# Performance work log

Measured on AMD Instinct MI355X. Metric: run time of the kernel, lower is better.

Reference implementation:

```python
import jax, jax.numpy as jnp
import numpy as np

S, B, D = 512, 256, 256

def _gelu(x):
    return jax.nn.gelu(x, approximate=False)  # torch nn.GELU default is exact erf

def _blacket(a, b, bl_w, bl_b):
    # GELU(Linear(cat([a,b], -1))); torch Linear: x @ W.T + b
    return _gelu(jnp.concatenate([a, b], axis=-1) @ bl_w.T + bl_b)

def setup_inputs() -> dict:
    key = jax.random.key(0)
    k1, k2, k3, k4, k5 = jax.random.split(key, 5)
    return {
        "src": jax.random.normal(k1, (S, B, D), dtype=jnp.float32),
        "map_w": jax.random.normal(k2, (D, D), dtype=jnp.float32) * (1.0 / np.sqrt(D)),
        "map_b": jax.random.normal(k3, (D,), dtype=jnp.float32) * 0.02,
        "bl_w": jax.random.normal(k4, (D, 2 * D), dtype=jnp.float32) * (1.0 / np.sqrt(2 * D)),
        "bl_b": jax.random.normal(k5, (D,), dtype=jnp.float32) * 0.02,
    }

def reference(src, map_w, map_b, bl_w, bl_b):
    # map_first: src <- GELU(Linear(src))
    h = _gelu(src @ map_w.T + map_b)          # [S, B, D]
    # base lie_func: x = h[i-1] (zeros at i=0), y = h[i]
    x = jnp.concatenate([jnp.zeros_like(h[:1]), h[:-1]], axis=0)
    delta = x + _blacket(x, h, bl_w, bl_b)    # [S, B, D]
    # jacobi identity for i >= 2 (note: torch `r += J` aliases context in base
    # mode, so J is folded into the carried context -> cumulative effect)
    a, b, c = h[:-2], h[1:-1], h[2:]          # [S-2, B, D]
    J = (_blacket(a, _blacket(b, c, bl_w, bl_b), bl_w, bl_b)
         + _blacket(b, _blacket(c, a, bl_w, bl_b), bl_w, bl_b)
         + _blacket(c, _blacket(a, b, bl_w, bl_b), bl_w, bl_b))
    total = delta.at[2:].add(J)
    return jnp.cumsum(total, axis=0)          # ret[i] = context_i (post-jacobi)
```

## Files before the change

kernel.cpp:

```cpp
#include <hip/hip_runtime.h>
#include <math.h>


typedef unsigned short u16;
typedef __attribute__((ext_vector_type(8))) short short8;
typedef __attribute__((ext_vector_type(4))) float floatx4;

#define DD 256
#define PSTR 264
#define NCOL 65536
#define SEGS 8

__device__ __forceinline__ float gelu_f(float v) {
    float u = 0.7978845608028654f * v * (1.0f + 0.044715f * v * v);
    float e = __expf(2.0f * u);
    float t = 1.0f - 2.0f * __builtin_amdgcn_rcpf(e + 1.0f);
    return 0.5f * v * (1.0f + t);
}
__device__ __forceinline__ u16 bf_bits(float f) {
    __bf16 b = (__bf16)f;
    return __builtin_bit_cast(unsigned short, b);
}
__device__ __forceinline__ float bf2f(u16 u) {
    unsigned int x = ((unsigned int)u) << 16;
    return __builtin_bit_cast(float, x);
}

__global__ __launch_bounds__(256) void fused_kernel(
    const u16* __restrict__ h, const u16* __restrict__ W,
    const float* __restrict__ bias, float* __restrict__ out)
{
    __shared__ u16 Alds[2][64 * 32];
    __shared__ u16 Wlds[2][256 * 32];
    __shared__ u16 Plds[64 * PSTR];

    const int tid = threadIdx.x;
    const int w = tid >> 6, lane = tid & 63;
    const int quad = lane >> 4, lr = lane & 15;
    const long m0 = (long)blockIdx.x * 64;
    const bool has_x = (m0 >= 256);
    const bool has_J = (m0 >= 512);
    const int st_row = lane >> 2;
    const int st_col = (lane & 3) * 8;

    float bias_r[4];
    #pragma unroll
    for (int j = 0; j < 4; ++j) bias_r[j] = bias[w * 64 + j * 16 + lr];

    floatx4 Jacc[4][4];
    floatx4 acc[4][4];

    auto zero_acc = [&](floatx4 (&a)[4][4]) {
        floatx4 z = {0.f, 0.f, 0.f, 0.f};
        #pragma unroll
        for (int i = 0; i < 4; ++i)
            #pragma unroll
            for (int j = 0; j < 4; ++j) a[i][j] = z;
    };

    auto stage = [&](int kt, int b, long r0, bool zero0, long r1, bool fromP) {
        const int k0 = kt * 32;
        if (k0 < 256) {
            if (zero0) {
                short8 z = {0, 0, 0, 0, 0, 0, 0, 0};
                *(short8*)&Alds[b][(w * 16 + st_row) * 32 + st_col] = z;
            } else {
                const long g = (r0 + w * 16 + st_row) * DD + k0 + st_col;
                __builtin_amdgcn_global_load_lds(
                    (const __attribute__((address_space(1))) unsigned int*)(h + g),
                    (__attribute__((address_space(3))) unsigned int*)(&Alds[b][w * 16 * 32]),
                    16, 0, 0);
            }
        } else if (!fromP) {
            const long g = (r1 + w * 16 + st_row) * DD + (k0 - 256) + st_col;
            __builtin_amdgcn_global_load_lds(
                (const __attribute__((address_space(1))) unsigned int*)(h + g),
                (__attribute__((address_space(3))) unsigned int*)(&Alds[b][w * 16 * 32]),
                16, 0, 0);
        }
        #pragma unroll
        for (int i = 0; i < 4; ++i) {
            const long g = (long)(w * 64 + i * 16 + st_row) * 512 + k0 + st_col;
            __builtin_amdgcn_global_load_lds(
                (const __attribute__((address_space(1))) unsigned int*)(W + g),
                (__attribute__((address_space(3))) unsigned int*)(&Wlds[b][(w * 64 + i * 16) * 32]),
                16, 0, 0);
        }
    };

    auto gemm_phase = [&](long r0, bool zero0, long r1, bool fromP) {
        stage(0, 0, r0, zero0, r1, fromP);
        for (int kt = 0; kt < 16; ++kt) {
            const int b = kt & 1;
            const int k0 = kt * 32;
            __syncthreads();
            short8 af[4], bfr[4];
            const bool rdP = fromP && (k0 >= 256);
            #pragma unroll
            for (int i = 0; i < 4; ++i) {
                if (rdP) af[i] = *(const short8*)&Plds[(i * 16 + lr) * PSTR + (k0 - 256) + quad * 8];
                else     af[i] = *(const short8*)&Alds[b][(i * 16 + lr) * 32 + quad * 8];
            }
            #pragma unroll
            for (int j = 0; j < 4; ++j)
                bfr[j] = *(const short8*)&Wlds[b][(w * 64 + j * 16 + lr) * 32 + quad * 8];
            if (kt < 15) stage(kt + 1, b ^ 1, r0, zero0, r1, fromP);
            #pragma unroll
            for (int i = 0; i < 4; ++i)
                #pragma unroll
                for (int j = 0; j < 4; ++j)
                    acc[i][j] = __builtin_amdgcn_mfma_f32_16x16x32_bf16(af[i], bfr[j], acc[i][j], 0, 0, 0);
        }
    };

    auto add_gelu = [&]() {
        #pragma unroll
        for (int j = 0; j < 4; ++j)
            #pragma unroll
            for (int i = 0; i < 4; ++i)
                #pragma unroll
                for (int r = 0; r < 4; ++r)
                    Jacc[i][j][r] += gelu_f(acc[i][j][r] + bias_r[j]);
    };
    auto write_P = [&]() {
        #pragma unroll
        for (int j = 0; j < 4; ++j) {
            const int n = w * 64 + j * 16 + lr;
            #pragma unroll
            for (int i = 0; i < 4; ++i)
                #pragma unroll
                for (int r = 0; r < 4; ++r)
                    Plds[(i * 16 + quad * 4 + r) * PSTR + n] =
                        bf_bits(gelu_f(acc[i][j][r] + bias_r[j]));
        }
    };

    zero_acc(acc);
    gemm_phase(m0 - 256, !has_x, m0, false);
    #pragma unroll
    for (int j = 0; j < 4; ++j) {
        const int n = w * 64 + j * 16 + lr;
        #pragma unroll
        for (int i = 0; i < 4; ++i) {
            const int rl = i * 16 + quad * 4;
            #pragma unroll
            for (int r = 0; r < 4; ++r) {
                float g = gelu_f(acc[i][j][r] + bias_r[j]);
                Plds[(rl + r) * PSTR + n] = bf_bits(g);
                float xv = has_x ? bf2f(h[(m0 - 256 + rl + r) * DD + n]) : 0.0f;
                Jacc[i][j][r] = g + xv;
            }
        }
    }

    if (has_J) {
        zero_acc(acc); gemm_phase(m0 - 512, false, 0, true);  add_gelu();
        zero_acc(acc); gemm_phase(m0, false, m0 - 512, false); write_P();
        zero_acc(acc); gemm_phase(m0 - 256, false, 0, true);  add_gelu();
        zero_acc(acc); gemm_phase(m0 - 512, false, m0 - 256, false); write_P();
        zero_acc(acc); gemm_phase(m0, false, 0, true);        add_gelu();
    }

    #pragma unroll
    for (int j = 0; j < 4; ++j) {
        const int n = w * 64 + j * 16 + lr;
        #pragma unroll
        for (int i = 0; i < 4; ++i) {
            const int rl = i * 16 + quad * 4;
            #pragma unroll
            for (int r = 0; r < 4; ++r)
                out[(m0 + rl + r) * DD + n] = Jacc[i][j][r];
        }
    }
}

__global__ __launch_bounds__(256) void h_gemm(
    const float* __restrict__ src, const u16* __restrict__ Wm,
    const float* __restrict__ bias, u16* __restrict__ hout)
{
    __shared__ u16 Alds[128 * 32];
    __shared__ u16 Blds[128 * 32];

    const int tid = threadIdx.x;
    const int bm = blockIdx.x * 128;
    const int bn = blockIdx.y * 128;
    const int w = tid >> 6, lane = tid & 63;
    const int quad = lane >> 4, lr = lane & 15;
    const int wm = (w & 1) * 64, wn = (w >> 1) * 64;

    floatx4 acc[4][4];
    {
        floatx4 z = {0.f, 0.f, 0.f, 0.f};
        #pragma unroll
        for (int i = 0; i < 4; ++i)
            #pragma unroll
            for (int j = 0; j < 4; ++j) acc[i][j] = z;
    }

    for (int k0 = 0; k0 < 256; k0 += 32) {
        __syncthreads();
        #pragma unroll
        for (int i = 0; i < 2; ++i) {
            const int row = w * 32 + i * 16 + (lane >> 2);
            const long g = (long)(bm + row) * DD + k0 + (lane & 3) * 8;
            floatx4 f0 = *(const floatx4*)(src + g);
            floatx4 f1 = *(const floatx4*)(src + g + 4);
            short8 v;
            #pragma unroll
            for (int e = 0; e < 4; ++e) {
                v[e]     = (short)bf_bits(f0[e]);
                v[e + 4] = (short)bf_bits(f1[e]);
            }
            *(short8*)&Alds[row * 32 + (lane & 3) * 8] = v;
        }
        #pragma unroll
        for (int i = 0; i < 2; ++i) {
            const int row = w * 32 + i * 16 + (lane >> 2);
            const long g = (long)(bn + row) * DD + k0 + (lane & 3) * 8;
            __builtin_amdgcn_global_load_lds(
                (const __attribute__((address_space(1))) unsigned int*)(Wm + g),
                (__attribute__((address_space(3))) unsigned int*)(Blds + (w * 32 + i * 16) * 32),
                16, 0, 0);
        }
        __syncthreads();

        short8 af[4], bfr[4];
        #pragma unroll
        for (int i = 0; i < 4; ++i)
            af[i] = *(const short8*)&Alds[(wm + i * 16 + lr) * 32 + quad * 8];
        #pragma unroll
        for (int j = 0; j < 4; ++j)
            bfr[j] = *(const short8*)&Blds[(wn + j * 16 + lr) * 32 + quad * 8];
        #pragma unroll
        for (int i = 0; i < 4; ++i)
            #pragma unroll
            for (int j = 0; j < 4; ++j)
                acc[i][j] = __builtin_amdgcn_mfma_f32_16x16x32_bf16(af[i], bfr[j], acc[i][j], 0, 0, 0);
    }

    #pragma unroll
    for (int j = 0; j < 4; ++j) {
        const int n = bn + wn + j * 16 + lr;
        const float bv = bias[n];
        #pragma unroll
        for (int i = 0; i < 4; ++i) {
            const int m = bm + wm + i * 16 + quad * 4;
            #pragma unroll
            for (int r = 0; r < 4; ++r)
                hout[(long)(m + r) * DD + n] = bf_bits(gelu_f(acc[i][j][r] + bv));
        }
    }
}

__global__ __launch_bounds__(256) void conv_w(const float* __restrict__ mw,
                                              const float* __restrict__ bw,
                                              u16* __restrict__ outw)
{
    const int i = blockIdx.x * 256 + threadIdx.x;
    outw[i] = (i < 65536) ? bf_bits(mw[i]) : bf_bits(bw[i - 65536]);
}

__global__ __launch_bounds__(256) void seg_sum_kernel(
    const float* __restrict__ out, float* __restrict__ sums)
{
    const int idx = blockIdx.x * 256 + threadIdx.x;
    const int seg = idx >> 16, col = idx & (NCOL - 1);
    const float* p = out + (long)seg * 64 * NCOL + col;
    float a = 0.f;
    #pragma unroll 8
    for (int s = 0; s < 64; ++s) a += p[(long)s * NCOL];
    sums[seg * NCOL + col] = a;
}

__global__ __launch_bounds__(256) void seg_offset_kernel(float* __restrict__ sums)
{
    const int col = blockIdx.x * 256 + threadIdx.x;
    float a = 0.f;
    #pragma unroll
    for (int g = 0; g < SEGS; ++g) {
        float v = sums[g * NCOL + col];
        sums[g * NCOL + col] = a;
        a += v;
    }
}

__global__ __launch_bounds__(256) void seg_apply_kernel(
    float* __restrict__ out, const float* __restrict__ sums)
{
    const int idx = blockIdx.x * 256 + threadIdx.x;
    const int seg = idx >> 16, col = idx & (NCOL - 1);
    float a = sums[seg * NCOL + col];
    float* p = out + (long)seg * 64 * NCOL + col;
    #pragma unroll 8
    for (int s = 0; s < 64; ++s) {
        a += p[(long)s * NCOL];
        p[(long)s * NCOL] = a;
    }
}

extern "C" void kernel_launch(void* const* d_in, const int* in_sizes, int n_in,
                              void* d_out, int out_size, void* d_ws, size_t ws_size,
                              hipStream_t stream)
{
    const float* src   = (const float*)d_in[0];
    const float* map_w = (const float*)d_in[1];
    const float* map_b = (const float*)d_in[2];
    const float* bl_w  = (const float*)d_in[3];
    const float* bl_b  = (const float*)d_in[4];
    float* out = (float*)d_out;

    const int SB = 512 * 256;

    u16* h_bf = (u16*)d_ws;
    u16* wbuf = h_bf + (long)SB * DD;
    u16* wmap = wbuf;
    u16* wbl  = wbuf + 65536;
    float* sums = (float*)(wbuf + 196608);

    const dim3 blk(256);

    conv_w<<<dim3(768), blk, 0, stream>>>(map_w, bl_w, wbuf);
    h_gemm<<<dim3(SB / 128, 2), blk, 0, stream>>>(src, wmap, map_b, h_bf);
    fused_kernel<<<dim3(SB / 64), blk, 0, stream>>>(h_bf, wbl, bl_b, out);
    seg_sum_kernel<<<dim3(SEGS * NCOL / 256), blk, 0, stream>>>(out, sums);
    seg_offset_kernel<<<dim3(NCOL / 256), blk, 0, stream>>>(sums);
    seg_apply_kernel<<<dim3(SEGS * NCOL / 256), blk, 0, stream>>>(out, sums);
}
```

Baseline: 867.7 us.

## Triple-buffer LDS staging with prefetch depth two and vmcnt-based waits

Replaces the double-buffered A/W LDS staging in the fused kernel with a three-stage ring that prefetches two k-tiles ahead. The per-iteration __syncthreads is replaced by an explicit s_waitcnt vmcnt plus s_barrier. To keep the outstanding-load count uniform for the vmcnt arithmetic, zero-fill and P-sourced stages now issue dummy global_load_lds into unused locations, and zero buffers are prefilled once up front. This aims to hide global load latency better, at the cost of more LDS, which may lower occupancy, and some redundant loads.

```diff
diff --git a/kernel.cpp b/kernel.cpp
--- a/kernel.cpp
+++ b/kernel.cpp
@@ -26,12 +26,15 @@
     return __builtin_bit_cast(float, x);
 }
 
+#define AS1(p) ((const __attribute__((address_space(1))) unsigned int*)(p))
+#define AS3(p) ((__attribute__((address_space(3))) unsigned int*)(p))
+
 __global__ __launch_bounds__(256) void fused_kernel(
     const u16* __restrict__ h, const u16* __restrict__ W,
     const float* __restrict__ bias, float* __restrict__ out)
 {
-    __shared__ u16 Alds[2][64 * 32];
-    __shared__ u16 Wlds[2][256 * 32];
+    __shared__ u16 Alds[3][64 * 32];
+    __shared__ u16 Wlds[3][256 * 32];
     __shared__ u16 Plds[64 * PSTR];
 
     const int tid = threadIdx.x;
@@ -58,42 +61,48 @@
             for (int j = 0; j < 4; ++j) a[i][j] = z;
     };
 
-    auto stage = [&](int kt, int b, long r0, bool zero0, long r1, bool fromP) {
-        const int k0 = kt * 32;
+    auto stage = [&](int s, long r0, bool zero0, long r1, bool fromP) {
+        const int k0 = s * 32;
+        const int b  = s % 3;
+        const u16* srcA;
+        u16* dstA;
         if (k0 < 256) {
             if (zero0) {
-                short8 z = {0, 0, 0, 0, 0, 0, 0, 0};
-                *(short8*)&Alds[b][(w * 16 + st_row) * 32 + st_col] = z;
+                srcA = h + (m0 + w * 16 + st_row) * DD + st_col;
+                dstA = Plds + w * 512;
             } else {
-                const long g = (r0 + w * 16 + st_row) * DD + k0 + st_col;
-                __builtin_amdgcn_global_load_lds(
-                    (const __attribute__((address_space(1))) unsigned int*)(h + g),
-                    (__attribute__((address_space(3))) unsigned int*)(&Alds[b][w * 16 * 32]),
-                    16, 0, 0);
+                srcA = h + (r0 + w * 16 + st_row) * DD + k0 + st_col;
+                dstA = &Alds[b][w * 16 * 32];
             }
-        } else if (!fromP) {
-            const long g = (r1 + w * 16 + st_row) * DD + (k0 - 256) + st_col;
-            __builtin_amdgcn_global_load_lds(
-                (const __attribute__((address_space(1))) unsigned int*)(h + g),
-                (__attribute__((address_space(3))) unsigned int*)(&Alds[b][w * 16 * 32]),
-                16, 0, 0);
-        }
+        } else if (fromP) {
+            srcA = h + (m0 + w * 16 + st_row) * DD + st_col;
+            dstA = &Alds[b][w * 16 * 32];
+        } else {
+            srcA = h + (r1 + w * 16 + st_row) * DD + (k0 - 256) + st_col;
+            dstA = &Alds[b][w * 16 * 32];
+        }
+        __builtin_amdgcn_global_load_lds(AS1(srcA), AS3(dstA), 16, 0, 0);
         #pragma unroll
         for (int i = 0; i < 4; ++i) {
             const long g = (long)(w * 64 + i * 16 + st_row) * 512 + k0 + st_col;
             __builtin_amdgcn_global_load_lds(
-                (const __attribute__((address_space(1))) unsigned int*)(W + g),
-                (__attribute__((address_space(3))) unsigned int*)(&Wlds[b][(w * 64 + i * 16) * 32]),
-                16, 0, 0);
+                AS1(W + g), AS3(&Wlds[b][(w * 64 + i * 16) * 32]), 16, 0, 0);
         }
     };
 
     auto gemm_phase = [&](long r0, bool zero0, long r1, bool fromP) {
-        stage(0, 0, r0, zero0, r1, fromP);
+        __syncthreads();
+        stage(0, r0, zero0, r1, fromP);
+        stage(1, r0, zero0, r1, fromP);
+        #pragma unroll
         for (int kt = 0; kt < 16; ++kt) {
-            const int b = kt & 1;
+            const int b = kt % 3;
             const int k0 = kt * 32;
-            __syncthreads();
+            if (kt < 15) asm volatile("s_waitcnt vmcnt(5)" ::: "memory");
+            else         asm volatile("s_waitcnt vmcnt(0)" ::: "memory");
+            __builtin_amdgcn_s_barrier();
+            __builtin_amdgcn_sched_barrier(0);
+            if (kt + 2 < 16) stage(kt + 2, r0, zero0, r1, fromP);
             short8 af[4], bfr[4];
             const bool rdP = fromP && (k0 >= 256);
             #pragma unroll
@@ -104,7 +113,6 @@
             #pragma unroll
             for (int j = 0; j < 4; ++j)
                 bfr[j] = *(const short8*)&Wlds[b][(w * 64 + j * 16 + lr) * 32 + quad * 8];
-            if (kt < 15) stage(kt + 1, b ^ 1, r0, zero0, r1, fromP);
             #pragma unroll
             for (int i = 0; i < 4; ++i)
                 #pragma unroll
@@ -134,6 +142,14 @@
                         bf_bits(gelu_f(acc[i][j][r] + bias_r[j]));
         }
     };
+
+    if (!has_x) {
+        short8 z = {0, 0, 0, 0, 0, 0, 0, 0};
+        #pragma unroll
+        for (int b = 0; b < 3; ++b)
+            *(short8*)&Alds[b][tid * 8] = z;
+        asm volatile("s_waitcnt lgkmcnt(0)" ::: "memory");
+    }
 
     zero_acc(acc);
     gemm_phase(m0 - 256, !has_x, m0, false);
@@ -154,11 +170,11 @@
     }
 
     if (has_J) {
-        zero_acc(acc); gemm_phase(m0 - 512, false, 0, true);  add_gelu();
-        zero_acc(acc); gemm_phase(m0, false, m0 - 512, false); write_P();
-        zero_acc(acc); gemm_phase(m0 - 256, false, 0, true);  add_gelu();
+        zero_acc(acc); gemm_phase(m0 - 512, false, m0, true);   add_gelu();
+        zero_acc(acc); gemm_phase(m0, false, m0 - 512, false);  write_P();
+        zero_acc(acc); gemm_phase(m0 - 256, false, m0, true);   add_gelu();
         zero_acc(acc); gemm_phase(m0 - 512, false, m0 - 256, false); write_P();
-        zero_acc(acc); gemm_phase(m0, false, 0, true);        add_gelu();
+        zero_acc(acc); gemm_phase(m0, false, m0, true);         add_gelu();
     }
 
     #pragma unroll
@@ -218,9 +234,7 @@
             const int row = w * 32 + i * 16 + (lane >> 2);
             const long g = (long)(bn + row) * DD + k0 + (lane & 3) * 8;
             __builtin_amdgcn_global_load_lds(
-                (const __attribute__((address_space(1))) unsigned int*)(Wm + g),
-                (__attribute__((address_space(3))) unsigned int*)(Blds + (w * 32 + i * 16) * 32),
-                16, 0, 0);
+                AS1(Wm + g), AS3(Blds + (w * 32 + i * 16) * 32), 16, 0, 0);
         }
         __syncthreads();
 
```

Measured after the change: 833.1 us. 4.0% less time.

## Batch three blacket GEMMs per phase to share weight tiles in fused kernel

Applied to the files above, without the earlier changes.

The fused kernel now computes three independent blacket GEMMs at once: delta plus the three inner brackets in the first pass, then the three outer brackets in a second pass. Each weight k-tile loaded into LDS feeds three accumulator sets, replacing six sequential GEMM phases that each reloaded the full weight matrix. The block grows to 512 threads in a 2x4 wave grid, and the bracket weight is pre-tiled into a k-major layout so staging loads are contiguous. This costs more LDS (three P buffers) and more accumulator registers, which may limit occupancy.

```diff
diff --git a/kernel.cpp b/kernel.cpp
--- a/kernel.cpp
+++ b/kernel.cpp
@@ -26,150 +26,171 @@
     return __builtin_bit_cast(float, x);
 }
 
-__global__ __launch_bounds__(256) void fused_kernel(
-    const u16* __restrict__ h, const u16* __restrict__ W,
+#define AS1(p) ((const __attribute__((address_space(1))) unsigned int*)(p))
+#define AS3(p) ((__attribute__((address_space(3))) unsigned int*)(p))
+
+__device__ __forceinline__ void gload(const u16* src, u16* dst) {
+    __builtin_amdgcn_global_load_lds(AS1(src), AS3(dst), 16, 0, 0);
+}
+
+__global__ __launch_bounds__(512, 2) void fused_kernel(
+    const u16* __restrict__ h, const u16* __restrict__ Wt,
     const float* __restrict__ bias, float* __restrict__ out)
 {
-    __shared__ u16 Alds[2][64 * 32];
-    __shared__ u16 Wlds[2][256 * 32];
-    __shared__ u16 Plds[64 * PSTR];
+    __shared__ u16 Ab[2][3][64 * 32];
+    __shared__ u16 Wb[2][256 * 32];
+    __shared__ u16 Pl[3][64 * PSTR];
 
     const int tid = threadIdx.x;
     const int w = tid >> 6, lane = tid & 63;
     const int quad = lane >> 4, lr = lane & 15;
+    const int wm = w >> 2, wn = w & 3;
     const long m0 = (long)blockIdx.x * 64;
     const bool has_x = (m0 >= 256);
     const bool has_J = (m0 >= 512);
-    const int st_row = lane >> 2;
-    const int st_col = (lane & 3) * 8;
+
+    const u16* hA0 = h + (has_J ? (m0 - 512) : m0) * DD;
+    const u16* hA1 = h + (has_x ? (m0 - 256) : m0) * DD;
+    const u16* hA2 = h + m0 * DD;
 
     float bias_r[4];
     #pragma unroll
-    for (int j = 0; j < 4; ++j) bias_r[j] = bias[w * 64 + j * 16 + lr];
-
-    floatx4 Jacc[4][4];
-    floatx4 acc[4][4];
-
-    auto zero_acc = [&](floatx4 (&a)[4][4]) {
+    for (int j = 0; j < 4; ++j) bias_r[j] = bias[wn * 64 + j * 16 + lr];
+
+    floatx4 acc0[2][4], acc1[2][4], acc2[2][4], Jacc[2][4];
+
+    auto zero3 = [&]() {
         floatx4 z = {0.f, 0.f, 0.f, 0.f};
         #pragma unroll
-        for (int i = 0; i < 4; ++i)
-            #pragma unroll
-            for (int j = 0; j < 4; ++j) a[i][j] = z;
+        for (int i = 0; i < 2; ++i)
+            #pragma unroll
+            for (int j = 0; j < 4; ++j) { acc0[i][j] = z; acc1[i][j] = z; acc2[i][j] = z; }
     };
 
-    auto stage = [&](int kt, int b, long r0, bool zero0, long r1, bool fromP) {
-        const int k0 = kt * 32;
-        if (k0 < 256) {
-            if (zero0) {
-                short8 z = {0, 0, 0, 0, 0, 0, 0, 0};
-                *(short8*)&Alds[b][(w * 16 + st_row) * 32 + st_col] = z;
-            } else {
-                const long g = (r0 + w * 16 + st_row) * DD + k0 + st_col;
-                __builtin_amdgcn_global_load_lds(
-                    (const __attribute__((address_space(1))) unsigned int*)(h + g),
-                    (__attribute__((address_space(3))) unsigned int*)(&Alds[b][w * 16 * 32]),
-                    16, 0, 0);
-            }
-        } else if (!fromP) {
-            const long g = (r1 + w * 16 + st_row) * DD + (k0 - 256) + st_col;
-            __builtin_amdgcn_global_load_lds(
-                (const __attribute__((address_space(1))) unsigned int*)(h + g),
-                (__attribute__((address_space(3))) unsigned int*)(&Alds[b][w * 16 * 32]),
-                16, 0, 0);
-        }
-        #pragma unroll
-        for (int i = 0; i < 4; ++i) {
-            const long g = (long)(w * 64 + i * 16 + st_row) * 512 + k0 + st_col;
-            __builtin_amdgcn_global_load_lds(
-                (const __attribute__((address_space(1))) unsigned int*)(W + g),
-                (__attribute__((address_space(3))) unsigned int*)(&Wlds[b][(w * 64 + i * 16) * 32]),
-                16, 0, 0);
+    auto stage = [&](int buf, int kt, bool withA) {
+        if (w < 4) {
+            #pragma unroll
+            for (int g = 0; g < 4; ++g) {
+                const int G = w * 4 + g;
+                gload(Wt + kt * 8192 + G * 512 + lane * 8, &Wb[buf][G * 512]);
+            }
+        } else if (withA) {
+            const int colq = (kt & 7) * 32;
+            #pragma unroll
+            for (int k = 0; k < 3; ++k) {
+                const int c = (w - 4) * 3 + k;
+                const int s = c >> 2, g = c & 3;
+                const u16* hs = (s == 0) ? hA0 : ((s == 1) ? hA1 : hA2);
+                gload(hs + (g * 16 + (lane >> 2)) * DD + colq + (lane & 3) * 8,
+                      &Ab[buf][0][0] + s * 2048 + g * 512);
+            }
         }
     };
 
-    auto gemm_phase = [&](long r0, bool zero0, long r1, bool fromP) {
-        stage(0, 0, r0, zero0, r1, fromP);
+    auto mma3 = [&](const u16* Abase, int rD, int rP2, int rP3,
+                    const u16* Wbase, bool zD) {
+        short8 bfr[4];
+        #pragma unroll
+        for (int j = 0; j < 4; ++j)
+            bfr[j] = *(const short8*)(Wbase + (wn * 64 + j * 16 + lr) * 32 + quad * 8);
+        #pragma unroll
+        for (int i = 0; i < 2; ++i) {
+            const int ro = (wm * 32 + i * 16 + lr) * 32 + quad * 8;
+            short8 a0 = *(const short8*)(Abase + rD * 2048 + ro);
+            short8 a1 = *(const short8*)(Abase + rP2 * 2048 + ro);
+            short8 a2 = *(const short8*)(Abase + rP3 * 2048 + ro);
+            if (zD) a0 = (short8){0, 0, 0, 0, 0, 0, 0, 0};
+            #pragma unroll
+            for (int j = 0; j < 4; ++j) {
+                acc0[i][j] = __builtin_amdgcn_mfma_f32_16x16x32_bf16(a0, bfr[j], acc0[i][j], 0, 0, 0);
+                acc1[i][j] = __builtin_amdgcn_mfma_f32_16x16x32_bf16(a1, bfr[j], acc1[i][j], 0, 0, 0);
+                acc2[i][j] = __builtin_amdgcn_mfma_f32_16x16x32_bf16(a2, bfr[j], acc2[i][j], 0, 0, 0);
+            }
+        }
+    };
+
+    auto mma3P = [&](const u16* Wbase, int colp) {
+        short8 bfr[4];
+        #pragma unroll
+        for (int j = 0; j < 4; ++j)
+            bfr[j] = *(const short8*)(Wbase + (wn * 64 + j * 16 + lr) * 32 + quad * 8);
+        #pragma unroll
+        for (int i = 0; i < 2; ++i) {
+            const int ro = (wm * 32 + i * 16 + lr) * PSTR + colp + quad * 8;
+            short8 a0 = *(const short8*)(&Pl[0][0] + ro);
+            short8 a1 = *(const short8*)(&Pl[1][0] + ro);
+            short8 a2 = *(const short8*)(&Pl[2][0] + ro);
+            #pragma unroll
+            for (int j = 0; j < 4; ++j) {
+                acc0[i][j] = __builtin_amdgcn_mfma_f32_16x16x32_bf16(a0, bfr[j], acc0[i][j], 0, 0, 0);
+                acc1[i][j] = __builtin_amdgcn_mfma_f32_16x16x32_bf16(a1, bfr[j], acc1[i][j], 0, 0, 0);
+                acc2[i][j] = __builtin_amdgcn_mfma_f32_16x16x32_bf16(a2, bfr[j], acc2[i][j], 0, 0, 0);
+            }
+        }
+    };
+
+    zero3();
+    stage(0, 0, true);
+    #pragma unroll
+    for (int kt = 0; kt < 16; ++kt) {
+        asm volatile("s_waitcnt vmcnt(0)" ::: "memory");
+        __builtin_amdgcn_s_barrier();
+        if (kt < 15) stage((kt + 1) & 1, kt + 1, true);
+        const bool lo = kt < 8;
+        mma3(&Ab[kt & 1][0][0], lo ? 1 : 2, lo ? 2 : 0, lo ? 0 : 1,
+             Wb[kt & 1], !has_x && lo);
+    }
+
+    if (has_J) stage(0, 0, true);
+
+    #pragma unroll
+    for (int j = 0; j < 4; ++j) {
+        const int n = wn * 64 + j * 16 + lr;
+        #pragma unroll
+        for (int i = 0; i < 2; ++i) {
+            const int rl = wm * 32 + i * 16 + quad * 4;
+            #pragma unroll
+            for (int r = 0; r < 4; ++r) {
+                float gD = gelu_f(acc0[i][j][r] + bias_r[j]);
+                float xv = has_x ? bf2f(h[(m0 - 256 + rl + r) * DD + n]) : 0.0f;
+                Jacc[i][j] [r] = gD + xv;
+                if (has_J) {
+                    Pl[0][(rl + r) * PSTR + n] = bf_bits(gD);
+                    Pl[1][(rl + r) * PSTR + n] = bf_bits(gelu_f(acc1[i][j][r] + bias_r[j]));
+                    Pl[2][(rl + r) * PSTR + n] = bf_bits(gelu_f(acc2[i][j][r] + bias_r[j]));
+                }
+            }
+        }
+    }
+    __syncthreads();
+
+    if (has_J) {
+        zero3();
+        #pragma unroll
         for (int kt = 0; kt < 16; ++kt) {
-            const int b = kt & 1;
-            const int k0 = kt * 32;
-            __syncthreads();
-            short8 af[4], bfr[4];
-            const bool rdP = fromP && (k0 >= 256);
-            #pragma unroll
-            for (int i = 0; i < 4; ++i) {
-                if (rdP) af[i] = *(const short8*)&Plds[(i * 16 + lr) * PSTR + (k0 - 256) + quad * 8];
-                else     af[i] = *(const short8*)&Alds[b][(i * 16 + lr) * 32 + quad * 8];
-            }
-            #pragma unroll
-            for (int j = 0; j < 4; ++j)
-                bfr[j] = *(const short8*)&Wlds[b][(w * 64 + j * 16 + lr) * 32 + quad * 8];
-            if (kt < 15) stage(kt + 1, b ^ 1, r0, zero0, r1, fromP);
-            #pragma unroll
-            for (int i = 0; i < 4; ++i)
-                #pragma unroll
-                for (int j = 0; j < 4; ++j)
-                    acc[i][j] = __builtin_amdgcn_mfma_f32_16x16x32_bf16(af[i], bfr[j], acc[i][j], 0, 0, 0);
-        }
-    };
-
-    auto add_gelu = [&]() {
-        #pragma unroll
-        for (int j = 0; j < 4; ++j)
-            #pragma unroll
-            for (int i = 0; i < 4; ++i)
-                #pragma unroll
-                for (int r = 0; r < 4; ++r)
-                    Jacc[i][j][r] += gelu_f(acc[i][j][r] + bias_r[j]);
-    };
-    auto write_P = [&]() {
-        #pragma unroll
-        for (int j = 0; j < 4; ++j) {
-            const int n = w * 64 + j * 16 + lr;
-            #pragma unroll
-            for (int i = 0; i < 4; ++i)
-                #pragma unroll
-                for (int r = 0; r < 4; ++r)
-                    Plds[(i * 16 + quad * 4 + r) * PSTR + n] =
-                        bf_bits(gelu_f(acc[i][j][r] + bias_r[j]));
-        }
-    };
-
-    zero_acc(acc);
-    gemm_phase(m0 - 256, !has_x, m0, false);
+            asm volatile("s_waitcnt vmcnt(0)" ::: "memory");
+            __builtin_amdgcn_s_barrier();
+            if (kt < 15) stage((kt + 1) & 1, kt + 1, (kt + 1) < 8);
+            if (kt < 8) mma3(&Ab[kt & 1][0][0], 0, 1, 2, Wb[kt & 1], false);
+            else        mma3P(Wb[kt & 1], (kt - 8) * 32);
+        }
+    }
+
     #pragma unroll
     for (int j = 0; j < 4; ++j) {
-        const int n = w * 64 + j * 16 + lr;
-        #pragma unroll
-        for (int i = 0; i < 4; ++i) {
-            const int rl = i * 16 + quad * 4;
+        const int n = wn * 64 + j * 16 + lr;
+        #pragma unroll
+        for (int i = 0; i < 2; ++i) {
+            const int rl = wm * 32 + i * 16 + quad * 4;
             #pragma unroll
             for (int r = 0; r < 4; ++r) {
-                float g = gelu_f(acc[i][j][r] + bias_r[j]);
-                Plds[(rl + r) * PSTR + n] = bf_bits(g);
-                float xv = has_x ? bf2f(h[(m0 - 256 + rl + r) * DD + n]) : 0.0f;
-                Jacc[i][j][r] = g + xv;
-            }
-        }
-    }
-
-    if (has_J) {
-        zero_acc(acc); gemm_phase(m0 - 512, false, 0, true);  add_gelu();
-        zero_acc(acc); gemm_phase(m0, false, m0 - 512, false); write_P();
-        zero_acc(acc); gemm_phase(m0 - 256, false, 0, true);  add_gelu();
-        zero_acc(acc); gemm_phase(m0 - 512, false, m0 - 256, false); write_P();
-        zero_acc(acc); gemm_phase(m0, false, 0, true);        add_gelu();
-    }
-
-    #pragma unroll
-    for (int j = 0; j < 4; ++j) {
-        const int n = w * 64 + j * 16 + lr;
-        #pragma unroll
-        for (int i = 0; i < 4; ++i) {
-            const int rl = i * 16 + quad * 4;
-            #pragma unroll
-            for (int r = 0; r < 4; ++r)
-                out[(m0 + rl + r) * DD + n] = Jacc[i][j][r];
+                float v = Jacc[i][j][r];
+                if (has_J)
+                    v += gelu_f(acc0[i][j][r] + bias_r[j])
+                       + gelu_f(acc1[i][j][r] + bias_r[j])
+                       + gelu_f(acc2[i][j][r] + bias_r[j]);
+                out[(m0 + rl + r) * DD + n] = v;
+            }
         }
     }
 }
@@ -218,9 +239,7 @@
             const int row = w * 32 + i * 16 + (lane >> 2);
             const long g = (long)(bn + row) * DD + k0 + (lane & 3) * 8;
             __builtin_amdgcn_global_load_lds(
-                (const __attribute__((address_space(1))) unsigned int*)(Wm + g),
-                (__attribute__((address_space(3))) unsigned int*)(Blds + (w * 32 + i * 16) * 32),
-                16, 0, 0);
+                AS1(Wm + g), AS3(Blds + (w * 32 + i * 16) * 32), 16, 0, 0);
         }
         __syncthreads();
 
@@ -257,7 +276,13 @@
                                               u16* __restrict__ outw)
 {
     const int i = blockIdx.x * 256 + threadIdx.x;
-    outw[i] = (i < 65536) ? bf_bits(mw[i]) : bf_bits(bw[i - 65536]);
+    if (i < 65536) {
+        outw[i] = bf_bits(mw[i]);
+    } else {
+        const int j = i - 65536;
+        const int n = j >> 9, k = j & 511;
+        outw[65536 + (k >> 5) * 8192 + n * 32 + (k & 31)] = bf_bits(bw[j]);
+    }
 }
 
 __global__ __launch_bounds__(256) void seg_sum_kernel(
@@ -321,7 +346,7 @@
 
     conv_w<<<dim3(768), blk, 0, stream>>>(map_w, bl_w, wbuf);
     h_gemm<<<dim3(SB / 128, 2), blk, 0, stream>>>(src, wmap, map_b, h_bf);
-    fused_kernel<<<dim3(SB / 64), blk, 0, stream>>>(h_bf, wbl, bl_b, out);
+    fused_kernel<<<dim3(SB / 64), dim3(512), 0, stream>>>(h_bf, wbl, bl_b, out);
     seg_sum_kernel<<<dim3(SEGS * NCOL / 256), blk, 0, stream>>>(out, sums);
     seg_offset_kernel<<<dim3(NCOL / 256), blk, 0, stream>>>(sums);
     seg_apply_kernel<<<dim3(SEGS * NCOL / 256), blk, 0, stream>>>(out, sums);
```

Result: faster. 838.3 us (-3.4%).
